# Kernel optimization log

Measured on AMD Instinct MI355X. Metric: run time of the kernel, lower is better.

The kernel has to match this reference:

```python
import jax, jax.numpy as jnp
import numpy as np
import math

S, B, H, NH = 2048, 1, 4096, 32
HD = H // NH          # 128 head dim
ROT = HD // 2         # 64 rotary dim per half (position_encoding_2d)


def _rotary_tables(seq_len):
    inv_freq = 1.0 / (10000.0 ** (jnp.arange(0, ROT, 2, dtype=jnp.float32) / ROT))  # [ROT/2]
    t = jnp.arange(seq_len, dtype=jnp.float32)
    freqs = jnp.einsum('i,j->ij', t, inv_freq)          # [S, ROT/2]
    emb = jnp.concatenate([freqs, freqs], axis=-1)       # [S, ROT]
    return jnp.cos(emb), jnp.sin(emb)


def _rotate_half(x):
    half = x.shape[-1] // 2
    return jnp.concatenate([-x[..., half:], x[..., :half]], axis=-1)


def _apply_rotary(q, k, cos, sin, pos):
    # q,k: [s,b,nh,ROT]; pos: [s,b]
    c = cos[pos][:, :, None, :]   # [s,b,1,ROT]
    s_ = sin[pos][:, :, None, :]
    return q * c + _rotate_half(q) * s_, k * c + _rotate_half(k) * s_


def reference(hidden_states, position_ids, attention_mask, layer_id, w_qkv, b_qkv, w_dense, b_dense):
    s, b, _ = hidden_states.shape
    # fused QKV projection (Linear: x @ W.T + b)
    qkv = jnp.einsum('sbh,oh->sbo', hidden_states, w_qkv) + b_qkv     # [s,b,3H]
    qkv = qkv.reshape(s, b, NH, 3 * HD)
    q, k, v = jnp.split(qkv, 3, axis=-1)                               # each [s,b,nh,HD]
    # 2D rotary: split head dim in two halves, rotate with pos / block pos ids
    cos, sin = _rotary_tables(s)
    pos = position_ids[:, 0, :].T        # [s,b]
    blk = position_ids[:, 1, :].T        # [s,b]
    q1, q2 = jnp.split(q, 2, axis=-1)
    k1, k2 = jnp.split(k, 2, axis=-1)
    q1, k1 = _apply_rotary(q1, k1, cos, sin, pos)
    q2, k2 = _apply_rotary(q2, k2, cos, sin, blk)
    q = jnp.concatenate([q1, q2], axis=-1)
    k = jnp.concatenate([k1, k2], axis=-1)
    # layer-id-dependent scaling (GLM numerics): q scaled down by coeff, logits scaled back up
    coeff = float(layer_id + 1)
    q = q / (math.sqrt(HD) * coeff)
    scores = jnp.einsum('sbnd,tbnd->bnst', q, k)                       # [b,nh,s,s]
    scores = jnp.where(attention_mask, jnp.asarray(-10000.0, scores.dtype), scores)
    probs = jax.nn.softmax(scores.astype(jnp.float32) * coeff, axis=-1).astype(scores.dtype)
    ctx = jnp.einsum('bnst,tbnd->sbnd', probs, v).reshape(s, b, H)     # [s,b,H]
    return jnp.einsum('sbh,oh->sbo', ctx, w_dense) + b_dense


def setup_inputs() -> dict:
    key = jax.random.key(0)
    k1, k2, k3, k4, k5, k6 = jax.random.split(key, 6)
    init = 0.02
    hidden_states = jax.random.normal(k1, (S, B, H), dtype=jnp.float32)
    # GLM-style 2D position ids: [B, 2, S] (row 0: positions, row 1: block positions)
    pos = jnp.broadcast_to(jnp.arange(S, dtype=jnp.int64), (B, S))
    blk = jnp.broadcast_to(jnp.arange(S, dtype=jnp.int64), (B, S))
    position_ids = jnp.stack([pos, blk], axis=1)                        # [B,2,S]
    # causal mask: True = masked (future positions)
    causal = jnp.triu(jnp.ones((S, S), dtype=bool), k=1)
    attention_mask = jnp.broadcast_to(causal[None, None], (B, 1, S, S))
    return {
        'hidden_states': hidden_states,
        'position_ids': position_ids,
        'attention_mask': attention_mask,
        'layer_id': 5,
        'w_qkv': jax.random.normal(k2, (3 * H, H), dtype=jnp.float32) * init,
        'b_qkv': jax.random.normal(k3, (3 * H,), dtype=jnp.float32) * init,
        'w_dense': jax.random.normal(k4, (H, H), dtype=jnp.float32) * init,
        'b_dense': jax.random.normal(k5, (H,), dtype=jnp.float32) * init,
    }
```

## Files before the change

### kernel.cpp

```cpp
#include <hip/hip_runtime.h>
#include <math.h>
#include <stdint.h>

constexpr int S  = 2048;
constexpr int H  = 4096;
constexpr int NH = 32;
constexpr int HD = 128;
constexpr int H3 = 3 * H;

typedef unsigned short u16;
typedef __bf16 bf16x8 __attribute__((ext_vector_type(8)));
typedef float  f32x4  __attribute__((ext_vector_type(4)));

__device__ __forceinline__ u16 f2bf(float f) {
  uint32_t u = __float_as_uint(f);
  uint32_t r = (u + 0x7fff + ((u >> 16) & 1)) >> 16;
  return (u16)r;
}
__device__ __forceinline__ float bf2f(u16 u) {
  return __uint_as_float((uint32_t)u << 16);
}

__device__ __forceinline__ void load_lds16(const void* g, void* l) {
  __builtin_amdgcn_global_load_lds(
      (__attribute__((address_space(1))) void*)(uintptr_t)g,
      (__attribute__((address_space(3))) void*)l,
      16, 0, 0);
}

#define SBAR0 __builtin_amdgcn_sched_barrier(0)

__global__ __launch_bounds__(256)
void castk(const float* __restrict__ in, u16* __restrict__ out, int n4) {
  for (int i = blockIdx.x * 256 + threadIdx.x; i < n4; i += gridDim.x * 256) {
    float4 v = ((const float4*)in)[i];
    ushort4 o;
    o.x = f2bf(v.x); o.y = f2bf(v.y); o.z = f2bf(v.z); o.w = f2bf(v.w);
    ((ushort4*)out)[i] = o;
  }
}

template<int NCOLS, int OUT_BF16>
__global__ __launch_bounds__(512, 2)
void gemm8p(const u16* __restrict__ A, const u16* __restrict__ W,
            const float* __restrict__ bias, void* __restrict__ Cout) {
  constexpr int K  = 4096;
  constexpr int NT = K / 64;
  constexpr int NTM = 16;
  constexpr int TB = 49152;
  __shared__ __attribute__((aligned(16))) unsigned char lds[3 * TB];
  const int tid = threadIdx.x, wave = tid >> 6, lane = tid & 63;
  const int l15 = lane & 15, l4 = lane >> 4;
  const int wr = wave >> 2, wc = wave & 3;

  const int nwg = gridDim.x, bid = blockIdx.x;
  const int cpx = nwg >> 3;
  const int swz = (bid & 7) * cpx + (bid >> 3);
  const int bx = swz / NTM, by = swz - bx * NTM;
  const int bm = by * 128, bn = bx * 256;

  const int srow = lane >> 3;
  const int sck  = ((lane & 7) ^ srow) * 8;
  const u16* Abase = A + (size_t)(bm + srow) * K + sck;
  const u16* Wbase = W + (size_t)(bn + srow) * K + sck;

  auto stageA = [&](int tt, int b) {
#pragma unroll
    for (int j = 0; j < 2; ++j) {
      const int rb = j * 64 + wave * 8;
      load_lds16(Abase + (size_t)rb * K + tt * 64, &lds[b * TB + rb * 128]);
    }
  };
  auto stageB = [&](int tt, int b, int u) {
#pragma unroll
    for (int j = 0; j < 2; ++j) {
      const int rb = u * 128 + j * 64 + wave * 8;
      load_lds16(Wbase + (size_t)rb * K + tt * 64,
                 &lds[b * TB + 16384 + rb * 128]);
    }
  };

  f32x4 acc[4][4];
#pragma unroll
  for (int i = 0; i < 4; ++i)
#pragma unroll
    for (int j = 0; j < 4; ++j) acc[i][j] = (f32x4)0.f;

  stageA(0, 0); stageB(0, 0, 0); stageB(0, 0, 1);
  stageA(1, 1); stageB(1, 1, 0); stageB(1, 1, 1);
  asm volatile("s_waitcnt vmcnt(6)" ::: "memory");
  SBAR0;
  __builtin_amdgcn_s_barrier();

  const int arow = wr * 64 + l15;
  const int brow = wc * 64 + l15;
  const int ckx  = l15 & 7;

  bf16x8 af[4][2], bf[4][2];

  int br = 0, bs = 2;
  for (int t = 0; t < NT; ++t) {
    const int b0 = br * TB;
#pragma unroll
    for (int mi = 0; mi < 2; ++mi)
#pragma unroll
      for (int ks = 0; ks < 2; ++ks)
        af[mi][ks] = *(const bf16x8*)&lds[b0 + (arow + mi * 16) * 128 +
                                          (((ks * 4 + l4) ^ ckx) * 16)];
#pragma unroll
    for (int ni = 0; ni < 2; ++ni)
#pragma unroll
      for (int ks = 0; ks < 2; ++ks)
        bf[ni][ks] = *(const bf16x8*)&lds[b0 + 16384 + (brow + ni * 16) * 128 +
                                          (((ks * 4 + l4) ^ ckx) * 16)];
    if (t < NT - 2) stageA(t + 2, bs);
    SBAR0; __builtin_amdgcn_s_barrier();
    asm volatile("s_waitcnt lgkmcnt(0)" ::: "memory");
    SBAR0;
    __builtin_amdgcn_s_setprio(1);
#pragma unroll
    for (int ks = 0; ks < 2; ++ks)
#pragma unroll
      for (int mi = 0; mi < 2; ++mi)
#pragma unroll
        for (int ni = 0; ni < 2; ++ni)
          acc[mi][ni] = __builtin_amdgcn_mfma_f32_16x16x32_bf16(af[mi][ks], bf[ni][ks], acc[mi][ni], 0, 0, 0);
    __builtin_amdgcn_s_setprio(0);
    SBAR0; __builtin_amdgcn_s_barrier();
#pragma unroll
    for (int ni = 2; ni < 4; ++ni)
#pragma unroll
      for (int ks = 0; ks < 2; ++ks)
        bf[ni][ks] = *(const bf16x8*)&lds[b0 + 16384 + (brow + ni * 16) * 128 +
                                          (((ks * 4 + l4) ^ ckx) * 16)];
    if (t < NT - 2) stageB(t + 2, bs, 0);
    SBAR0; __builtin_amdgcn_s_barrier();
    asm volatile("s_waitcnt lgkmcnt(0)" ::: "memory");
    SBAR0;
    __builtin_amdgcn_s_setprio(1);
#pragma unroll
    for (int ks = 0; ks < 2; ++ks)
#pragma unroll
      for (int mi = 0; mi < 2; ++mi)
#pragma unroll
        for (int ni = 2; ni < 4; ++ni)
          acc[mi][ni] = __builtin_amdgcn_mfma_f32_16x16x32_bf16(af[mi][ks], bf[ni][ks], acc[mi][ni], 0, 0, 0);
    __builtin_amdgcn_s_setprio(0);
    SBAR0; __builtin_amdgcn_s_barrier();
#pragma unroll
    for (int mi = 2; mi < 4; ++mi)
#pragma unroll
      for (int ks = 0; ks < 2; ++ks)
        af[mi][ks] = *(const bf16x8*)&lds[b0 + (arow + mi * 16) * 128 +
                                          (((ks * 4 + l4) ^ ckx) * 16)];
    if (t < NT - 2) stageB(t + 2, bs, 1);
    SBAR0; __builtin_amdgcn_s_barrier();
    asm volatile("s_waitcnt lgkmcnt(0)" ::: "memory");
    SBAR0;
    __builtin_amdgcn_s_setprio(1);
#pragma unroll
    for (int ks = 0; ks < 2; ++ks)
#pragma unroll
      for (int mi = 2; mi < 4; ++mi)
#pragma unroll
        for (int ni = 0; ni < 2; ++ni)
          acc[mi][ni] = __builtin_amdgcn_mfma_f32_16x16x32_bf16(af[mi][ks], bf[ni][ks], acc[mi][ni], 0, 0, 0);
    __builtin_amdgcn_s_setprio(0);
    SBAR0; __builtin_amdgcn_s_barrier();
    __builtin_amdgcn_s_setprio(1);
#pragma unroll
    for (int ks = 0; ks < 2; ++ks)
#pragma unroll
      for (int mi = 2; mi < 4; ++mi)
#pragma unroll
        for (int ni = 2; ni < 4; ++ni)
          acc[mi][ni] = __builtin_amdgcn_mfma_f32_16x16x32_bf16(af[mi][ks], bf[ni][ks], acc[mi][ni], 0, 0, 0);
    __builtin_amdgcn_s_setprio(0);
    if (t < NT - 1) {
      if (t < NT - 2) asm volatile("s_waitcnt vmcnt(6)" ::: "memory");
      else            asm volatile("s_waitcnt vmcnt(0)" ::: "memory");
      SBAR0;
      __builtin_amdgcn_s_barrier();
    }
    br = (br == 2) ? 0 : br + 1;
    bs = (bs == 2) ? 0 : bs + 1;
  }

#pragma unroll
  for (int ni = 0; ni < 4; ++ni) {
    const int col = bn + wc * 64 + ni * 16 + l15;
    const float bv = bias[col];
#pragma unroll
    for (int mi = 0; mi < 4; ++mi) {
#pragma unroll
      for (int r = 0; r < 4; ++r) {
        const int row = bm + wr * 64 + mi * 16 + l4 * 4 + r;
        const float v = acc[mi][ni][r] + bv;
        if (OUT_BF16) ((u16*)Cout)[(size_t)row * NCOLS + col] = f2bf(v);
        else          ((float*)Cout)[(size_t)row * NCOLS + col] = v;
      }
    }
  }
}

__global__ __launch_bounds__(128)
void rotary(const u16* __restrict__ qkv, u16* __restrict__ Qb, u16* __restrict__ Kb) {
  const int s = blockIdx.x, h = blockIdx.y, d = threadIdx.x;
  const u16* base = qkv + (size_t)s * H3 + h * 384;
  const float qv = bf2f(base[d]);
  const float kv = bf2f(base[128 + d]);
  const float qp = bf2f(base[d ^ 32]);
  const float kp = bf2f(base[128 + (d ^ 32)]);
  const int dd = d & 63, j = dd & 31;
  const float invf = exp2f(-(float)j * (13.287712379549449f / 32.f));
  float sn, c;
  sincosf((float)s * invf, &sn, &c);
  const float sign = (dd < 32) ? -1.f : 1.f;
  const float qo = qv * c + sign * qp * sn;
  const float ko = kv * c + sign * kp * sn;
  const size_t o = ((size_t)h * S + s) * HD + d;
  Qb[o] = f2bf(qo * 0.12751721769218683f);
  Kb[o] = f2bf(ko);
}

__global__ __launch_bounds__(256)
void transpose_v(const u16* __restrict__ qkv, u16* __restrict__ Vt) {
  __shared__ u16 tile[64][130];
  const int s0 = blockIdx.x * 64, h = blockIdx.y;
  for (int idx = threadIdx.x; idx < 64 * 128; idx += 256) {
    const int r = idx >> 7, c = idx & 127;
    tile[r][c] = qkv[(size_t)(s0 + r) * H3 + h * 384 + 256 + c];
  }
  __syncthreads();
  for (int idx = threadIdx.x; idx < 128 * 64; idx += 256) {
    const int d = idx >> 6, c = idx & 63;
    Vt[((size_t)h * HD + d) * S + s0 + c] = tile[c][d];
  }
}

__global__ __launch_bounds__(256)
void attn(const u16* __restrict__ Qb, const u16* __restrict__ Kb,
          const u16* __restrict__ Vt, u16* __restrict__ ctx) {
  __shared__ __attribute__((aligned(16))) unsigned char sK[64 * 256];
  __shared__ __attribute__((aligned(16))) unsigned char sV[128 * 128];
  __shared__ __attribute__((aligned(16))) unsigned char sP[4][16 * 128];
  const int qb = blockIdx.x, h = blockIdx.y;
  const int tid = threadIdx.x, wave = tid >> 6, lane = tid & 63;
  const int l15 = lane & 15, l4 = lane >> 4;
  const int qw0 = qb * 64 + wave * 16;

  bf16x8 qf[4];
  {
    const u16* qrow = Qb + ((size_t)h * S + qw0 + l15) * HD;
#pragma unroll
    for (int ks = 0; ks < 4; ++ks)
      qf[ks] = *(const bf16x8*)(qrow + ks * 32 + l4 * 8);
  }

  f32x4 of[8];
#pragma unroll
  for (int i = 0; i < 8; ++i) of[i] = (f32x4)0.f;
  float mrun[4] = {-1e30f, -1e30f, -1e30f, -1e30f};
  float lrun[4] = {0.f, 0.f, 0.f, 0.f};

  const int nt = qb + 1;
  for (int it = 0; it < nt; ++it) {
    const int t0 = it * 64;
#pragma unroll
    for (int c = 0; c < 4; ++c) {
      const int rbase = c * 16 + wave * 4;
      const int rr = rbase + (lane >> 4);
      const int p = lane & 15;
      load_lds16(Kb + ((size_t)h * S + t0 + rr) * HD + ((p ^ (rr & 15)) * 8),
                 &sK[rbase * 256]);
    }
#pragma unroll
    for (int c = 0; c < 4; ++c) {
      const int rbase = c * 32 + wave * 8;
      const int rr = rbase + (lane >> 3);
      const int p = lane & 7;
      load_lds16(Vt + ((size_t)h * HD + rr) * S + t0 + ((p ^ (rr & 7)) * 8),
                 &sV[rbase * 128]);
    }
    __syncthreads();

    f32x4 sc[4];
#pragma unroll
    for (int nf = 0; nf < 4; ++nf) sc[nf] = (f32x4)0.f;
#pragma unroll
    for (int nf = 0; nf < 4; ++nf) {
      const int trow = nf * 16 + l15;
#pragma unroll
      for (int ks = 0; ks < 4; ++ks) {
        const int chunk = ks * 4 + l4;
        bf16x8 kf = *(const bf16x8*)&sK[trow * 256 + ((chunk ^ (trow & 15)) * 16)];
        sc[nf] = __builtin_amdgcn_mfma_f32_16x16x32_bf16(qf[ks], kf, sc[nf], 0, 0, 0);
      }
    }

    if (t0 == qb * 64) {
#pragma unroll
      for (int nf = 0; nf < 4; ++nf) {
        const int tg = t0 + nf * 16 + l15;
#pragma unroll
        for (int r = 0; r < 4; ++r) {
          const int sg = qw0 + l4 * 4 + r;
          if (tg > sg) sc[nf][r] = -1e30f;
        }
      }
    }

    f32x4 vm = sc[0];
#pragma unroll
    for (int nf = 1; nf < 4; ++nf)
#pragma unroll
      for (int r = 0; r < 4; ++r) vm[r] = fmaxf(vm[r], sc[nf][r]);
#pragma unroll
    for (int m = 1; m <= 8; m <<= 1)
#pragma unroll
      for (int r = 0; r < 4; ++r) vm[r] = fmaxf(vm[r], __shfl_xor(vm[r], m, 64));

    float scale[4];
#pragma unroll
    for (int r = 0; r < 4; ++r) {
      const float nm = fmaxf(mrun[r], vm[r]);
      scale[r] = exp2f(mrun[r] - nm);
      mrun[r] = nm;
    }

    f32x4 rs = (f32x4)0.f;
#pragma unroll
    for (int nf = 0; nf < 4; ++nf) {
#pragma unroll
      for (int r = 0; r < 4; ++r) {
        const float p = exp2f(sc[nf][r] - mrun[r]);
        rs[r] += p;
        const int row = l4 * 4 + r;
        const int t = nf * 16 + l15;
        const int chunk = t >> 3;
        *(u16*)&sP[wave][row * 128 + ((chunk ^ (row & 7)) * 16) + (t & 7) * 2] = f2bf(p);
      }
    }
#pragma unroll
    for (int m = 1; m <= 8; m <<= 1)
#pragma unroll
      for (int r = 0; r < 4; ++r) rs[r] += __shfl_xor(rs[r], m, 64);
#pragma unroll
    for (int r = 0; r < 4; ++r) lrun[r] = lrun[r] * scale[r] + rs[r];
#pragma unroll
    for (int i = 0; i < 8; ++i)
#pragma unroll
      for (int r = 0; r < 4; ++r) of[i][r] *= scale[r];

    asm volatile("s_waitcnt lgkmcnt(0)" ::: "memory");
    __builtin_amdgcn_sched_barrier(0);

    bf16x8 pa[2];
#pragma unroll
    for (int ksP = 0; ksP < 2; ++ksP) {
      const int chunk = ksP * 4 + l4;
      pa[ksP] = *(const bf16x8*)&sP[wave][l15 * 128 + ((chunk ^ (l15 & 7)) * 16)];
    }
#pragma unroll
    for (int nf2 = 0; nf2 < 8; ++nf2) {
      const int d = nf2 * 16 + l15;
#pragma unroll
      for (int ksP = 0; ksP < 2; ++ksP) {
        const int chunk = ksP * 4 + l4;
        bf16x8 vf = *(const bf16x8*)&sV[d * 128 + ((chunk ^ (d & 7)) * 16)];
        of[nf2] = __builtin_amdgcn_mfma_f32_16x16x32_bf16(pa[ksP], vf, of[nf2], 0, 0, 0);
      }
    }
    __syncthreads();
  }

  float invr[4];
#pragma unroll
  for (int r = 0; r < 4; ++r) invr[r] = 1.f / lrun[r];
#pragma unroll
  for (int nf2 = 0; nf2 < 8; ++nf2) {
    const int d = nf2 * 16 + l15;
#pragma unroll
    for (int r = 0; r < 4; ++r) {
      const int srow = qw0 + l4 * 4 + r;
      ctx[(size_t)srow * H + h * HD + d] = f2bf(of[nf2][r] * invr[r]);
    }
  }
}

extern "C" void kernel_launch(void* const* d_in, const int* in_sizes, int n_in,
                              void* d_out, int out_size, void* d_ws, size_t ws_size,
                              hipStream_t stream) {
  (void)in_sizes; (void)n_in; (void)out_size; (void)ws_size;
  const float* hidden  = (const float*)d_in[0];
  const float* w_qkv   = (const float*)d_in[4];
  const float* b_qkv   = (const float*)d_in[5];
  const float* w_dense = (const float*)d_in[6];
  const float* b_dense = (const float*)d_in[7];
  float* out = (float*)d_out;

  char* ws = (char*)d_ws;
  u16* wqkvb   = (u16*)(ws + 0);
  u16* wdenseb = (u16*)(ws + 0);
  u16* ctxb    = (u16*)(ws + 41943040);
  u16* hb      = (u16*)(ws + 100663296);
  u16* qkvb    = (u16*)(ws + 117440512);
  u16* Qbp     = (u16*)(ws + 167772160);
  u16* Kbp     = (u16*)(ws + 184549376);
  u16* Vtp     = (u16*)(ws + 201326592);

  castk<<<2048, 256, 0, stream>>>(w_qkv, wqkvb, (H3 * H) / 4);
  castk<<<2048, 256, 0, stream>>>(hidden, hb, (S * H) / 4);
  gemm8p<H3, 1><<<dim3(768), 512, 0, stream>>>(hb, wqkvb, b_qkv, qkvb);
  rotary<<<dim3(S, NH), 128, 0, stream>>>(qkvb, Qbp, Kbp);
  transpose_v<<<dim3(S / 64, NH), 256, 0, stream>>>(qkvb, Vtp);
  castk<<<2048, 256, 0, stream>>>(w_dense, wdenseb, (H * H) / 4);
  attn<<<dim3(S / 64, NH), 256, 0, stream>>>(Qbp, Kbp, Vtp, ctxb);
  gemm8p<H, 0><<<dim3(256), 512, 0, stream>>>(ctxb, wdenseb, b_dense, out);
}
```

Before: 535.6 us.

## Use 256x256-tile double-buffered GEMM for the QKV projection

Adds a new bf16 MFMA GEMM kernel with 256x256 output tiles, a two-stage LDS double buffer (128KB), and global loads interleaved across four MFMA quarter-phases. It replaces the earlier 3-buffer kernel for the QKV projection, halving the grid to 384 workgroups. Larger tiles raise arithmetic intensity and cut global/L2 traffic per FLOP. The cost is a shallower pipeline, heavier register use, and fewer workgroups per CU (256 CUs get 384 tiles, so there is a wave-quantization tail).

```diff
diff --git a/kernel.cpp b/kernel.cpp
--- a/kernel.cpp
+++ b/kernel.cpp
@@ -37,6 +37,164 @@
     ushort4 o;
     o.x = f2bf(v.x); o.y = f2bf(v.y); o.z = f2bf(v.z); o.w = f2bf(v.w);
     ((ushort4*)out)[i] = o;
+  }
+}
+
+template<int NCOLS, int OUT_BF16>
+__global__ __launch_bounds__(512, 2)
+void gemm256(const u16* __restrict__ A, const u16* __restrict__ W,
+             const float* __restrict__ bias, void* __restrict__ Cout) {
+  constexpr int K   = 4096;
+  constexpr int NT  = K / 64;
+  constexpr int NTM = 8;
+  constexpr int TB  = 65536;
+  __shared__ __attribute__((aligned(16))) unsigned char lds[2 * TB];
+  const int tid = threadIdx.x, wave = tid >> 6, lane = tid & 63;
+  const int l15 = lane & 15, l4 = lane >> 4;
+  const int wr = wave >> 2, wc = wave & 3;
+
+  const int nwg = gridDim.x, bid = blockIdx.x;
+  const int cpx = nwg >> 3;
+  const int swz = (bid & 7) * cpx + (bid >> 3);
+  const int bx = swz / NTM, by = swz - bx * NTM;
+  const int bm = by * 256, bn = bx * 256;
+
+  const int srow = lane >> 3;
+  const int sck  = ((lane & 7) ^ srow) * 8;
+  const u16* Abase = A + (size_t)(bm + srow) * K + sck;
+  const u16* Wbase = W + (size_t)(bn + srow) * K + sck;
+
+  auto stageU = [&](int tt, int u) {
+    const int b = tt & 1;
+    if (u < 4) {
+      const int rb = u * 64 + wave * 8;
+      load_lds16(Abase + (size_t)rb * K + tt * 64, &lds[b * TB + rb * 128]);
+    } else {
+      const int rb = (u - 4) * 64 + wave * 8;
+      load_lds16(Wbase + (size_t)rb * K + tt * 64,
+                 &lds[b * TB + 32768 + rb * 128]);
+    }
+  };
+
+  f32x4 acc[8][4];
+#pragma unroll
+  for (int i = 0; i < 8; ++i)
+#pragma unroll
+    for (int j = 0; j < 4; ++j) acc[i][j] = (f32x4)0.f;
+
+#pragma unroll
+  for (int u = 0; u < 8; ++u) stageU(0, u);
+#pragma unroll
+  for (int u = 0; u < 8; ++u) stageU(1, u);
+  asm volatile("s_waitcnt vmcnt(8)" ::: "memory");
+  SBAR0;
+  __builtin_amdgcn_s_barrier();
+
+  const int arow = wr * 128 + l15;
+  const int brow = wc * 64 + l15;
+  const int ckx  = l15 & 7;
+
+  bf16x8 af[4][2], bfA[2][2], bfB[2][2];
+
+  for (int t = 0; t < NT; ++t) {
+    const int b0 = (t & 1) * TB;
+    const bool st = (t + 2 < NT);
+#pragma unroll
+    for (int mi = 0; mi < 4; ++mi)
+#pragma unroll
+      for (int ks = 0; ks < 2; ++ks)
+        af[mi][ks] = *(const bf16x8*)&lds[b0 + (arow + mi * 16) * 128 +
+                                          (((ks * 4 + l4) ^ ckx) * 16)];
+#pragma unroll
+    for (int ni = 0; ni < 2; ++ni)
+#pragma unroll
+      for (int ks = 0; ks < 2; ++ks)
+        bfA[ni][ks] = *(const bf16x8*)&lds[b0 + 32768 + (brow + ni * 16) * 128 +
+                                           (((ks * 4 + l4) ^ ckx) * 16)];
+    SBAR0; __builtin_amdgcn_s_barrier();
+    asm volatile("s_waitcnt lgkmcnt(0)" ::: "memory");
+    SBAR0;
+    __builtin_amdgcn_s_setprio(1);
+#pragma unroll
+    for (int ks = 0; ks < 2; ++ks)
+#pragma unroll
+      for (int mi = 0; mi < 4; ++mi)
+#pragma unroll
+        for (int ni = 0; ni < 2; ++ni)
+          acc[mi][ni] = __builtin_amdgcn_mfma_f32_16x16x32_bf16(af[mi][ks], bfA[ni][ks], acc[mi][ni], 0, 0, 0);
+    __builtin_amdgcn_s_setprio(0);
+    SBAR0; __builtin_amdgcn_s_barrier();
+#pragma unroll
+    for (int ni = 0; ni < 2; ++ni)
+#pragma unroll
+      for (int ks = 0; ks < 2; ++ks)
+        bfB[ni][ks] = *(const bf16x8*)&lds[b0 + 32768 + (brow + (ni + 2) * 16) * 128 +
+                                           (((ks * 4 + l4) ^ ckx) * 16)];
+    if (st) { stageU(t + 2, 0); stageU(t + 2, 2); }
+    SBAR0; __builtin_amdgcn_s_barrier();
+    asm volatile("s_waitcnt lgkmcnt(0)" ::: "memory");
+    SBAR0;
+    __builtin_amdgcn_s_setprio(1);
+#pragma unroll
+    for (int ks = 0; ks < 2; ++ks)
+#pragma unroll
+      for (int mi = 0; mi < 4; ++mi)
+#pragma unroll
+        for (int ni = 0; ni < 2; ++ni)
+          acc[mi][ni + 2] = __builtin_amdgcn_mfma_f32_16x16x32_bf16(af[mi][ks], bfB[ni][ks], acc[mi][ni + 2], 0, 0, 0);
+    __builtin_amdgcn_s_setprio(0);
+    SBAR0; __builtin_amdgcn_s_barrier();
+#pragma unroll
+    for (int mi = 0; mi < 4; ++mi)
+#pragma unroll
+      for (int ks = 0; ks < 2; ++ks)
+        af[mi][ks] = *(const bf16x8*)&lds[b0 + (arow + (mi + 4) * 16) * 128 +
+                                          (((ks * 4 + l4) ^ ckx) * 16)];
+    if (st) { stageU(t + 2, 4); stageU(t + 2, 5); }
+    SBAR0; __builtin_amdgcn_s_barrier();
+    asm volatile("s_waitcnt lgkmcnt(0)" ::: "memory");
+    SBAR0;
+    __builtin_amdgcn_s_setprio(1);
+#pragma unroll
+    for (int ks = 0; ks < 2; ++ks)
+#pragma unroll
+      for (int mi = 0; mi < 4; ++mi)
+#pragma unroll
+        for (int ni = 0; ni < 2; ++ni)
+          acc[mi + 4][ni] = __builtin_amdgcn_mfma_f32_16x16x32_bf16(af[mi][ks], bfA[ni][ks], acc[mi + 4][ni], 0, 0, 0);
+    __builtin_amdgcn_s_setprio(0);
+    SBAR0; __builtin_amdgcn_s_barrier();
+    if (st) { stageU(t + 2, 1); stageU(t + 2, 3); stageU(t + 2, 6); stageU(t + 2, 7); }
+    SBAR0;
+    __builtin_amdgcn_s_setprio(1);
+#pragma unroll
+    for (int ks = 0; ks < 2; ++ks)
+#pragma unroll
+      for (int mi = 0; mi < 4; ++mi)
+#pragma unroll
+        for (int ni = 0; ni < 2; ++ni)
+          acc[mi + 4][ni + 2] = __builtin_amdgcn_mfma_f32_16x16x32_bf16(af[mi][ks], bfB[ni][ks], acc[mi + 4][ni + 2], 0, 0, 0);
+    __builtin_amdgcn_s_setprio(0);
+    if (t < NT - 2)       asm volatile("s_waitcnt vmcnt(8)" ::: "memory");
+    else if (t == NT - 2) asm volatile("s_waitcnt vmcnt(0)" ::: "memory");
+    SBAR0;
+    if (t < NT - 1) __builtin_amdgcn_s_barrier();
+  }
+
+#pragma unroll
+  for (int ni = 0; ni < 4; ++ni) {
+    const int col = bn + wc * 64 + ni * 16 + l15;
+    const float bv = bias[col];
+#pragma unroll
+    for (int mi = 0; mi < 8; ++mi) {
+#pragma unroll
+      for (int r = 0; r < 4; ++r) {
+        const int row = bm + wr * 128 + mi * 16 + l4 * 4 + r;
+        const float v = acc[mi][ni][r] + bv;
+        if (OUT_BF16) ((u16*)Cout)[(size_t)row * NCOLS + col] = f2bf(v);
+        else          ((float*)Cout)[(size_t)row * NCOLS + col] = v;
+      }
+    }
   }
 }
 
@@ -411,7 +569,7 @@
 
   castk<<<2048, 256, 0, stream>>>(w_qkv, wqkvb, (H3 * H) / 4);
   castk<<<2048, 256, 0, stream>>>(hidden, hb, (S * H) / 4);
-  gemm8p<H3, 1><<<dim3(768), 512, 0, stream>>>(hb, wqkvb, b_qkv, qkvb);
+  gemm256<H3, 1><<<dim3(384), 512, 0, stream>>>(hb, wqkvb, b_qkv, qkvb);
   rotary<<<dim3(S, NH), 128, 0, stream>>>(qkvb, Qbp, Kbp);
   transpose_v<<<dim3(S / 64, NH), 256, 0, stream>>>(qkvb, Vtp);
   castk<<<2048, 256, 0, stream>>>(w_dense, wdenseb, (H * H) / 4);
```

Result: slower. 554.8 us (+3.6%).

## Double-buffer K/V tiles in attention and fuse rotary with V transpose

Applied to the files above, without the earlier changes.

The attention kernel now keeps two LDS buffers for K and V and issues the async global-to-LDS loads for the next tile before computing the current one. It waits with vmcnt and raw s_barrier in place of full __syncthreads, so load latency can overlap with the MFMA and softmax work. The separate rotary and V-transpose kernels are merged into one kernel that precomputes a sin/cos table per 64-row tile and uses 16-byte vector loads and stores, removing a launch and the scalar accesses. LDS use in attention roughly doubles, which may reduce occupancy.

```diff
diff --git a/kernel.cpp b/kernel.cpp
--- a/kernel.cpp
+++ b/kernel.cpp
@@ -11,6 +11,7 @@
 typedef unsigned short u16;
 typedef __bf16 bf16x8 __attribute__((ext_vector_type(8)));
 typedef float  f32x4  __attribute__((ext_vector_type(4)));
+typedef unsigned short us8 __attribute__((ext_vector_type(8)));
 
 __device__ __forceinline__ u16 f2bf(float f) {
   uint32_t u = __float_as_uint(f);
@@ -203,76 +204,78 @@
   }
 }
 
-__global__ __launch_bounds__(128)
-void rotary(const u16* __restrict__ qkv, u16* __restrict__ Qb, u16* __restrict__ Kb) {
-  const int s = blockIdx.x, h = blockIdx.y, d = threadIdx.x;
-  const u16* base = qkv + (size_t)s * H3 + h * 384;
-  const float qv = bf2f(base[d]);
-  const float kv = bf2f(base[128 + d]);
-  const float qp = bf2f(base[d ^ 32]);
-  const float kp = bf2f(base[128 + (d ^ 32)]);
-  const int dd = d & 63, j = dd & 31;
-  const float invf = exp2f(-(float)j * (13.287712379549449f / 32.f));
-  float sn, c;
-  sincosf((float)s * invf, &sn, &c);
-  const float sign = (dd < 32) ? -1.f : 1.f;
-  const float qo = qv * c + sign * qp * sn;
-  const float ko = kv * c + sign * kp * sn;
-  const size_t o = ((size_t)h * S + s) * HD + d;
-  Qb[o] = f2bf(qo * 0.12751721769218683f);
-  Kb[o] = f2bf(ko);
-}
-
 __global__ __launch_bounds__(256)
-void transpose_v(const u16* __restrict__ qkv, u16* __restrict__ Vt) {
-  __shared__ u16 tile[64][130];
+void rotary_fused(const u16* __restrict__ qkv,
+                  u16* __restrict__ Qb, u16* __restrict__ Kb,
+                  u16* __restrict__ Vt) {
+  __shared__ u16 vt[64][136];
+  __shared__ float2 cs_tab[64][32];
   const int s0 = blockIdx.x * 64, h = blockIdx.y;
-  for (int idx = threadIdx.x; idx < 64 * 128; idx += 256) {
-    const int r = idx >> 7, c = idx & 127;
-    tile[r][c] = qkv[(size_t)(s0 + r) * H3 + h * 384 + 256 + c];
+  const int tid = threadIdx.x;
+
+  for (int idx = tid; idx < 2048; idx += 256) {
+    const int r = idx >> 5, j = idx & 31;
+    const float invf = exp2f(-(float)j * (13.287712379549449f / 32.f));
+    float sn, c;
+    sincosf((float)(s0 + r) * invf, &sn, &c);
+    cs_tab[r][j] = make_float2(c, sn);
+  }
+  for (int idx = tid; idx < 1024; idx += 256) {
+    const int r = idx >> 4, ck = idx & 15;
+    us8 v = *(const us8*)(qkv + (size_t)(s0 + r) * H3 + h * 384 + 256 + ck * 8);
+    *(us8*)&vt[r][ck * 8] = v;
   }
   __syncthreads();
-  for (int idx = threadIdx.x; idx < 128 * 64; idx += 256) {
-    const int d = idx >> 6, c = idx & 63;
-    Vt[((size_t)h * HD + d) * S + s0 + c] = tile[c][d];
+
+  for (int idx = tid; idx < 2048; idx += 256) {
+    const int r  = idx >> 5;
+    const int sub = idx & 31;
+    const int tq = sub >> 4;
+    const int ck = sub & 15;
+    const int s = s0 + r;
+    const u16* base = qkv + (size_t)s * H3 + h * 384 + tq * 128;
+    us8 v = *(const us8*)(base + ck * 8);
+    us8 p = *(const us8*)(base + ((ck * 8) ^ 32));
+    const int d0 = ck * 8;
+    const float sign = ((d0 & 63) < 32) ? -1.f : 1.f;
+    const float sc = tq ? 1.f : 0.12751721769218683f;
+    us8 o;
+#pragma unroll
+    for (int e = 0; e < 8; ++e) {
+      const float2 cs = cs_tab[r][(d0 + e) & 31];
+      o[e] = f2bf((bf2f(v[e]) * cs.x + sign * bf2f(p[e]) * cs.y) * sc);
+    }
+    *(us8*)((tq ? Kb : Qb) + ((size_t)h * S + s) * HD + d0) = o;
+  }
+  for (int idx = tid; idx < 1024; idx += 256) {
+    const int d = idx >> 3, c8 = idx & 7;
+    us8 o;
+#pragma unroll
+    for (int e = 0; e < 8; ++e) o[e] = vt[c8 * 8 + e][d];
+    *(us8*)(Vt + ((size_t)h * HD + d) * S + s0 + c8 * 8) = o;
   }
 }
 
 __global__ __launch_bounds__(256)
 void attn(const u16* __restrict__ Qb, const u16* __restrict__ Kb,
           const u16* __restrict__ Vt, u16* __restrict__ ctx) {
-  __shared__ __attribute__((aligned(16))) unsigned char sK[64 * 256];
-  __shared__ __attribute__((aligned(16))) unsigned char sV[128 * 128];
+  __shared__ __attribute__((aligned(16))) unsigned char sK[2][64 * 256];
+  __shared__ __attribute__((aligned(16))) unsigned char sV[2][128 * 128];
   __shared__ __attribute__((aligned(16))) unsigned char sP[4][16 * 128];
   const int qb = blockIdx.x, h = blockIdx.y;
   const int tid = threadIdx.x, wave = tid >> 6, lane = tid & 63;
   const int l15 = lane & 15, l4 = lane >> 4;
   const int qw0 = qb * 64 + wave * 16;
 
-  bf16x8 qf[4];
-  {
-    const u16* qrow = Qb + ((size_t)h * S + qw0 + l15) * HD;
-#pragma unroll
-    for (int ks = 0; ks < 4; ++ks)
-      qf[ks] = *(const bf16x8*)(qrow + ks * 32 + l4 * 8);
-  }
-
-  f32x4 of[8];
-#pragma unroll
-  for (int i = 0; i < 8; ++i) of[i] = (f32x4)0.f;
-  float mrun[4] = {-1e30f, -1e30f, -1e30f, -1e30f};
-  float lrun[4] = {0.f, 0.f, 0.f, 0.f};
-
-  const int nt = qb + 1;
-  for (int it = 0; it < nt; ++it) {
-    const int t0 = it * 64;
+  auto stage = [&](int it) {
+    const int t0 = it * 64, b = it & 1;
 #pragma unroll
     for (int c = 0; c < 4; ++c) {
       const int rbase = c * 16 + wave * 4;
       const int rr = rbase + (lane >> 4);
       const int p = lane & 15;
       load_lds16(Kb + ((size_t)h * S + t0 + rr) * HD + ((p ^ (rr & 15)) * 8),
-                 &sK[rbase * 256]);
+                 &sK[b][rbase * 256]);
     }
 #pragma unroll
     for (int c = 0; c < 4; ++c) {
@@ -280,9 +283,37 @@
       const int rr = rbase + (lane >> 3);
       const int p = lane & 7;
       load_lds16(Vt + ((size_t)h * HD + rr) * S + t0 + ((p ^ (rr & 7)) * 8),
-                 &sV[rbase * 128]);
-    }
-    __syncthreads();
+                 &sV[b][rbase * 128]);
+    }
+  };
+
+  bf16x8 qf[4];
+  {
+    const u16* qrow = Qb + ((size_t)h * S + qw0 + l15) * HD;
+#pragma unroll
+    for (int ks = 0; ks < 4; ++ks)
+      qf[ks] = *(const bf16x8*)(qrow + ks * 32 + l4 * 8);
+  }
+
+  f32x4 of[8];
+#pragma unroll
+  for (int i = 0; i < 8; ++i) of[i] = (f32x4)0.f;
+  float mrun[4] = {-1e30f, -1e30f, -1e30f, -1e30f};
+  float lrun[4] = {0.f, 0.f, 0.f, 0.f};
+
+  const int nt = qb + 1;
+  stage(0);
+  for (int it = 0; it < nt; ++it) {
+    const int t0 = it * 64, b = it & 1;
+    if (it + 1 < nt) {
+      stage(it + 1);
+      asm volatile("s_waitcnt vmcnt(8)" ::: "memory");
+    } else {
+      asm volatile("s_waitcnt vmcnt(0)" ::: "memory");
+    }
+    SBAR0;
+    __builtin_amdgcn_s_barrier();
+    SBAR0;
 
     f32x4 sc[4];
 #pragma unroll
@@ -293,12 +324,12 @@
 #pragma unroll
       for (int ks = 0; ks < 4; ++ks) {
         const int chunk = ks * 4 + l4;
-        bf16x8 kf = *(const bf16x8*)&sK[trow * 256 + ((chunk ^ (trow & 15)) * 16)];
+        bf16x8 kf = *(const bf16x8*)&sK[b][trow * 256 + ((chunk ^ (trow & 15)) * 16)];
         sc[nf] = __builtin_amdgcn_mfma_f32_16x16x32_bf16(qf[ks], kf, sc[nf], 0, 0, 0);
       }
     }
 
-    if (t0 == qb * 64) {
+    if (it == qb) {
 #pragma unroll
       for (int nf = 0; nf < 4; ++nf) {
         const int tg = t0 + nf * 16 + l15;
@@ -353,7 +384,7 @@
       for (int r = 0; r < 4; ++r) of[i][r] *= scale[r];
 
     asm volatile("s_waitcnt lgkmcnt(0)" ::: "memory");
-    __builtin_amdgcn_sched_barrier(0);
+    SBAR0;
 
     bf16x8 pa[2];
 #pragma unroll
@@ -367,11 +398,12 @@
 #pragma unroll
       for (int ksP = 0; ksP < 2; ++ksP) {
         const int chunk = ksP * 4 + l4;
-        bf16x8 vf = *(const bf16x8*)&sV[d * 128 + ((chunk ^ (d & 7)) * 16)];
+        bf16x8 vf = *(const bf16x8*)&sV[b][d * 128 + ((chunk ^ (d & 7)) * 16)];
         of[nf2] = __builtin_amdgcn_mfma_f32_16x16x32_bf16(pa[ksP], vf, of[nf2], 0, 0, 0);
       }
     }
-    __syncthreads();
+    SBAR0;
+    __builtin_amdgcn_s_barrier();
   }
 
   float invr[4];
@@ -412,8 +444,7 @@
   castk<<<2048, 256, 0, stream>>>(w_qkv, wqkvb, (H3 * H) / 4);
   castk<<<2048, 256, 0, stream>>>(hidden, hb, (S * H) / 4);
   gemm8p<H3, 1><<<dim3(768), 512, 0, stream>>>(hb, wqkvb, b_qkv, qkvb);
-  rotary<<<dim3(S, NH), 128, 0, stream>>>(qkvb, Qbp, Kbp);
-  transpose_v<<<dim3(S / 64, NH), 256, 0, stream>>>(qkvb, Vtp);
+  rotary_fused<<<dim3(S / 64, NH), 256, 0, stream>>>(qkvb, Qbp, Kbp, Vtp);
   castk<<<2048, 256, 0, stream>>>(w_dense, wdenseb, (H * H) / 4);
   attn<<<dim3(S / 64, NH), 256, 0, stream>>>(Qbp, Kbp, Vtp, ctxb);
   gemm8p<H, 0><<<dim3(256), 512, 0, stream>>>(ctxb, wdenseb, b_dense, out);
```

New measurement: 522.8 us. 1.02x faster.
